# Performance work log

Hardware: AMD Instinct MI355X
Metric: run time of the kernel (lower is better)

Reference implementation:

```python
import jax, jax.numpy as jnp
import numpy as np


def setup_inputs() -> dict:
    key = jax.random.key(0)
    k1, k2, k3 = jax.random.split(key, 3)
    B, S, D, N = 2, 2048, 1024, 16
    H = D // N  # head_dim = 64
    x = jax.random.normal(k1, (B, S, D), dtype=jnp.float32)
    W_qkv = jax.random.normal(k2, (N, D, 3 * H), dtype=jnp.float32) / np.sqrt(D).astype(np.float32)
    W_out = jax.random.normal(k3, (N, H, D), dtype=jnp.float32) / np.sqrt(D).astype(np.float32)
    return {"x": x, "W_qkv": W_qkv, "W_out": W_out}


def reference(x, W_qkv, W_out):
    B, S, D = x.shape
    head_dim = W_qkv.shape[-1] // 3
    # QKV projection per head: [B, N, S, 3*H]
    qkv = jnp.einsum('bsd,ndh->bnsh', x, W_qkv)
    q, k, v = jnp.split(qkv, 3, axis=-1)  # each [B, N, S, H]
    scale = jnp.asarray(1.0 / np.sqrt(head_dim), dtype=x.dtype)
    attn = jnp.einsum('bnqh,bnkh->bnqk', q, k) * scale  # [B, N, S, S]
    # causal mask: -1e10 above the diagonal (matches buffer in original)
    mask = jnp.asarray(-1e10, dtype=x.dtype) * (1.0 - jnp.tril(jnp.ones((S, S), dtype=x.dtype)))
    attn = jax.nn.softmax(attn + mask, axis=-1)
    out = jnp.einsum('bnqk,bnkh->bnqh', attn, v)  # [B, N, S, H]
    # faithful to original: raw row-major reshape [B,N,S,H] -> [B, N*H, S]
    out = out.reshape(B, -1, S)
    # faithful to original einsum: d kept, n and h summed over W_out
    return jnp.einsum('bds,nhd->bsd', out, W_out)
```

## Files before the change

kernel.cpp:

```cpp
#include <hip/hip_runtime.h>
#include <hip/hip_bf16.h>

#define B_ 2
#define S_ 2048
#define D_ 1024
#define N_ 16
#define H_ 64

typedef unsigned short u16;
typedef unsigned int u32;
typedef __bf16 bf16x8 __attribute__((ext_vector_type(8)));
typedef u16 u16x8 __attribute__((ext_vector_type(8)));
typedef u32 u32x2 __attribute__((ext_vector_type(2)));
typedef u32 u32x4 __attribute__((ext_vector_type(4)));
typedef float f4v __attribute__((ext_vector_type(4)));

__device__ __forceinline__ u16 f2b(float f) {
    u32 u = __builtin_bit_cast(u32, f);
    u32 r = (u + 0x7FFFu + ((u >> 16) & 1u)) >> 16;
    return (u16)r;
}
__device__ __forceinline__ bf16x8 asbf(u16x8 v) { return __builtin_bit_cast(bf16x8, v); }
__device__ __forceinline__ u32 cvtpk(float a, float b) {
    u32 r;
    asm("v_cvt_pk_bf16_f32 %0, %1, %2" : "=v"(r) : "v"(a), "v"(b));
    return r;
}
__device__ __forceinline__ void gload16(const u16* g, u16* l) {
    __builtin_amdgcn_global_load_lds((const __attribute__((address_space(1))) void*)g,
                                     (__attribute__((address_space(3))) void*)l, 16, 0, 0);
}

__global__ __launch_bounds__(256) void k_setup(const float* __restrict__ x,
                                               const float* __restrict__ w,
                                               const float* __restrict__ Wout,
                                               u16* __restrict__ xb,
                                               u16* __restrict__ wt,
                                               float* __restrict__ wsum) {
    __shared__ float T[64][65];
    const int bid = blockIdx.x;
    const int t = threadIdx.x;
    if (bid < 2048) {
        size_t i = ((size_t)bid * 256 + t) * 8;
        float4 f0 = *(const float4*)(x + i);
        float4 f1 = *(const float4*)(x + i + 4);
        u16x8 o;
        o[0] = f2b(f0.x); o[1] = f2b(f0.y); o[2] = f2b(f0.z); o[3] = f2b(f0.w);
        o[4] = f2b(f1.x); o[5] = f2b(f1.y); o[6] = f2b(f1.z); o[7] = f2b(f1.w);
        *(u16x8*)(xb + i) = o;
    } else if (bid < 2816) {
        const int v = bid - 2048;
        const int n = v / 48, rem = v % 48;
        const int jt = rem >> 4, d0 = (rem & 15) * 64;
        const int j0 = jt * 64;
        const float sc = (jt == 0) ? 0.125f * 1.44269504089f : 1.0f;
#pragma unroll
        for (int rep = 0; rep < 4; ++rep) {
            int vv = t + rep * 256;
            int row = vv >> 4, c4 = vv & 15;
            float4 f = *(const float4*)(w + ((size_t)(n * 1024 + d0 + row)) * 192 + j0 + c4 * 4);
            T[row][c4 * 4 + 0] = f.x * sc;
            T[row][c4 * 4 + 1] = f.y * sc;
            T[row][c4 * 4 + 2] = f.z * sc;
            T[row][c4 * 4 + 3] = f.w * sc;
        }
        __syncthreads();
#pragma unroll
        for (int rep = 0; rep < 2; ++rep) {
            int c = t + rep * 256;
            int j = c >> 3, db = c & 7;
            u16x8 o;
#pragma unroll
            for (int e = 0; e < 8; ++e) o[e] = f2b(T[db * 8 + e][j]);
            *(u16x8*)(wt + ((size_t)(n * 192 + j0 + j)) * 1024 + d0 + db * 8) = o;
        }
    } else {
        const int bx = bid - 2816;
        const int dd = t & 15, rr = t >> 4;
        const int d = bx * 16 + dd;
        float s = 0.f;
        for (int r = rr * 64; r < rr * 64 + 64; ++r) s += Wout[(size_t)r * 1024 + d];
        float* red = &T[0][0];
        red[rr * 17 + dd] = s;
        __syncthreads();
        if (rr == 0) {
            float tt = 0.f;
#pragma unroll
            for (int k = 0; k < 16; ++k) tt += red[k * 17 + dd];
            wsum[d] = tt;
        }
    }
}

__global__ __launch_bounds__(512) void k_qkv(const u16* __restrict__ xb,
                                             const u16* __restrict__ wt,
                                             u16* __restrict__ qbuf,
                                             u16* __restrict__ kbuf,
                                             u16* __restrict__ vt) {
    __shared__ u16 As[128 * 64];
    __shared__ u16 Bst[192 * 64];
    const int st = blockIdx.x, n = blockIdx.y;
    const int t = threadIdx.x;
    const int w = t >> 6, lane = t & 63, hi2 = lane >> 4, lo4 = lane & 15;
    const int wm = w >> 2, wn = w & 3;

    const int l8 = lane >> 3, l7 = (lane & 7) * 8;
    const u16* AgL = xb + (size_t)(st * 128 + w * 16 + l8) * 1024 + l7;
    u16* AdL = As + w * 16 * 64;
    const u16* BgL = wt + (size_t)(n * 192 + w * 24 + l8) * 1024 + l7;
    u16* BdL = Bst + w * 24 * 64;

    f4v acc[4][3];
#pragma unroll
    for (int i = 0; i < 4; ++i)
#pragma unroll
        for (int j = 0; j < 3; ++j) acc[i][j] = (f4v){0.f, 0.f, 0.f, 0.f};

    for (int kk = 0; kk < 16; ++kk) {
        __syncthreads();
        const int ko = kk * 64;
        gload16(AgL + ko, AdL);
        gload16(AgL + ko + (size_t)8 * 1024, AdL + 8 * 64);
        gload16(BgL + ko, BdL);
        gload16(BgL + ko + (size_t)8 * 1024, BdL + 8 * 64);
        gload16(BgL + ko + (size_t)16 * 1024, BdL + 16 * 64);
        __syncthreads();
        bf16x8 fa[4][2];
#pragma unroll
        for (int ms = 0; ms < 4; ++ms) {
            const u16* ar = As + (wm * 64 + ms * 16 + lo4) * 64;
            fa[ms][0] = asbf(*(const u16x8*)(ar + hi2 * 8));
            fa[ms][1] = asbf(*(const u16x8*)(ar + hi2 * 8 + 32));
        }
        __builtin_amdgcn_s_setprio(1);
#pragma unroll
        for (int fj = 0; fj < 3; ++fj) {
            const u16* br = Bst + (wn * 48 + fj * 16 + lo4) * 64;
            bf16x8 fb0 = asbf(*(const u16x8*)(br + hi2 * 8));
            bf16x8 fb1 = asbf(*(const u16x8*)(br + hi2 * 8 + 32));
#pragma unroll
            for (int ms = 0; ms < 4; ++ms) {
                acc[ms][fj] = __builtin_amdgcn_mfma_f32_16x16x32_bf16(fa[ms][0], fb0, acc[ms][fj], 0, 0, 0);
                acc[ms][fj] = __builtin_amdgcn_mfma_f32_16x16x32_bf16(fa[ms][1], fb1, acc[ms][fj], 0, 0, 0);
            }
        }
        __builtin_amdgcn_s_setprio(0);
    }

    const int b = st >> 4, s128 = (st & 15) * 128;
    u16* Cs = As;
#pragma unroll
    for (int sec = 0; sec < 3; ++sec) {
        __syncthreads();
#pragma unroll
        for (int fj = 0; fj < 3; ++fj) {
            const int base = wn * 48 + fj * 16;
            if ((base >> 6) == sec) {
                const int col = base - sec * 64 + lo4;
#pragma unroll
                for (int ms = 0; ms < 4; ++ms)
#pragma unroll
                    for (int r = 0; r < 4; ++r)
                        Cs[(wm * 64 + ms * 16 + hi2 * 4 + r) * 64 + col] = f2b(acc[ms][fj][r]);
            }
        }
        __syncthreads();
        if (sec == 2) {
            const int h = t & 63, sb = t >> 6;
            u16x8 o0, o1;
#pragma unroll
            for (int e = 0; e < 8; ++e) o0[e] = Cs[(sb * 16 + e) * 64 + h];
#pragma unroll
            for (int e = 0; e < 8; ++e) o1[e] = Cs[(sb * 16 + 8 + e) * 64 + h];
            u16* dst = vt + ((size_t)(b * 16 + n) * 64 + h) * 2048 + s128 + sb * 16;
            *(u16x8*)dst = o0;
            *(u16x8*)(dst + 8) = o1;
        } else {
            const int row = t >> 2, off = (t & 3) * 16;
            u16* dst = (sec == 0) ? qbuf : kbuf;
            dst += ((size_t)(b * 16 + n) * 2048 + s128 + row) * 64 + off;
            *(u16x8*)dst = *(const u16x8*)(Cs + row * 64 + off);
            *(u16x8*)(dst + 8) = *(const u16x8*)(Cs + row * 64 + off + 8);
        }
    }
}

__global__ __launch_bounds__(512) void k_attn(const u16* __restrict__ qbuf,
                                              const u16* __restrict__ kbuf,
                                              const u16* __restrict__ vt,
                                              const float* __restrict__ wsum,
                                              float* __restrict__ out) {
    __shared__ u16 SMEM[16384];
    u16* Ks = SMEM;
    u16* Vs = SMEM + 8192;
    const int id = blockIdx.x;
    const int bn = id & 31;
    const int qx = id >> 5;
    const int qb = (qx < 8) ? (15 - 2 * qx) : (2 * (qx - 8));
    const int t = threadIdx.x;
    const int w = t >> 6, lane = t & 63, hi2 = lane >> 4, lo4 = lane & 15;

    const int q = qb * 128 + w * 16 + lo4;
    const u16* Qp = qbuf + ((size_t)bn * 2048 + q) * 64;
    bf16x8 bq0 = asbf(*(const u16x8*)(Qp + hi2 * 8));
    bf16x8 bq1 = asbf(*(const u16x8*)(Qp + 32 + hi2 * 8));

    const int srow = t >> 3, so = t & 7;
    const u16* Kg = kbuf + (size_t)bn * 2048 * 64 + (size_t)srow * 64 + so * 8;
    const u16* Vg = vt + (size_t)bn * 64 * 2048 + (size_t)srow * 2048 + so * 8;
    const int ssw = (srow & 7) << 3;
    const int ksoff = srow * 64 + ((so * 8) ^ ssw);
    const int vsb = 32 * (so >> 2) + 16 * (so & 1) + 4 * ((so >> 1) & 1);
    const int vo0 = srow * 64 + ((vsb + 0) ^ ssw);
    const int vo1 = srow * 64 + ((vsb + 8) ^ ssw);

    f4v accO[4];
#pragma unroll
    for (int i = 0; i < 4; ++i) accO[i] = (f4v){0.f, 0.f, 0.f, 0.f};
    float l = 0.f;

    const int rsw = (lo4 & 7) << 3;
    const int npair = qb + 1;

    u16x8 krA = *(const u16x8*)(Kg);
    u16x8 krB = *(const u16x8*)(Kg + 4096);
    u16x8 vrA = *(const u16x8*)(Vg);
    u16x8 vrB = *(const u16x8*)(Vg + 64);

    for (int pair = 0; pair < npair; ++pair) {
        __syncthreads();
        *(u16x8*)(Ks + ksoff) = krA;
        *(u16x8*)(Ks + 4096 + ksoff) = krB;
        {
            u32x4 va = __builtin_bit_cast(u32x4, vrA);
            u32x4 vb = __builtin_bit_cast(u32x4, vrB);
            *(u32x2*)(Vs + vo0) = (u32x2){va[0], va[1]};
            *(u32x2*)(Vs + vo1) = (u32x2){va[2], va[3]};
            *(u32x2*)(Vs + 4096 + vo0) = (u32x2){vb[0], vb[1]};
            *(u32x2*)(Vs + 4096 + vo1) = (u32x2){vb[2], vb[3]};
        }
        if (pair + 1 < npair) {
            const size_t ko = (size_t)(pair + 1) * 8192;
            krA = *(const u16x8*)(Kg + ko);
            krB = *(const u16x8*)(Kg + ko + 4096);
            vrA = *(const u16x8*)(Vg + (pair + 1) * 128);
            vrB = *(const u16x8*)(Vg + (pair + 1) * 128 + 64);
        }
        __syncthreads();

#pragma unroll
        for (int sub = 0; sub < 2; ++sub) {
            const int kb = 2 * pair + sub;
            const u16* Kc = Ks + sub * 4096;
            const u16* Vc = Vs + sub * 4096;

            f4v s4[4];
#pragma unroll
            for (int i = 0; i < 4; ++i) s4[i] = (f4v){0.f, 0.f, 0.f, 0.f};
            __builtin_amdgcn_s_setprio(1);
#pragma unroll
            for (int fi = 0; fi < 4; ++fi) {
                const u16* kr = Kc + (fi * 16 + lo4) * 64;
                bf16x8 ka0 = asbf(*(const u16x8*)(kr + ((hi2 * 8) ^ rsw)));
                bf16x8 ka1 = asbf(*(const u16x8*)(kr + ((hi2 * 8 + 32) ^ rsw)));
                s4[fi] = __builtin_amdgcn_mfma_f32_16x16x32_bf16(ka0, bq0, s4[fi], 0, 0, 0);
                s4[fi] = __builtin_amdgcn_mfma_f32_16x16x32_bf16(ka1, bq1, s4[fi], 0, 0, 0);
            }
            __builtin_amdgcn_s_setprio(0);

            if (kb >= 2 * qb) {
#pragma unroll
                for (int fi = 0; fi < 4; ++fi)
#pragma unroll
                    for (int r = 0; r < 4; ++r) {
                        int kvg = kb * 64 + fi * 16 + hi2 * 4 + r;
                        if (kvg > q) s4[fi][r] = -3.0e38f;
                    }
            }

#pragma unroll
            for (int fi = 0; fi < 4; ++fi)
#pragma unroll
                for (int r = 0; r < 4; ++r) {
                    float pv = __builtin_exp2f(s4[fi][r]);
                    s4[fi][r] = pv;
                    l += pv;
                }

            u32x4 p0 = {cvtpk(s4[0][0], s4[0][1]), cvtpk(s4[0][2], s4[0][3]),
                        cvtpk(s4[1][0], s4[1][1]), cvtpk(s4[1][2], s4[1][3])};
            u32x4 p1 = {cvtpk(s4[2][0], s4[2][1]), cvtpk(s4[2][2], s4[2][3]),
                        cvtpk(s4[3][0], s4[3][1]), cvtpk(s4[3][2], s4[3][3])};
            bf16x8 pb0 = __builtin_bit_cast(bf16x8, p0);
            bf16x8 pb1 = __builtin_bit_cast(bf16x8, p1);

            __builtin_amdgcn_s_setprio(1);
#pragma unroll
            for (int fh = 0; fh < 4; ++fh) {
                const u16* vrw = Vc + (fh * 16 + lo4) * 64;
                bf16x8 va0 = asbf(*(const u16x8*)(vrw + ((hi2 * 8) ^ rsw)));
                bf16x8 va1 = asbf(*(const u16x8*)(vrw + ((32 + hi2 * 8) ^ rsw)));
                accO[fh] = __builtin_amdgcn_mfma_f32_16x16x32_bf16(va0, pb0, accO[fh], 0, 0, 0);
                accO[fh] = __builtin_amdgcn_mfma_f32_16x16x32_bf16(va1, pb1, accO[fh], 0, 0, 0);
            }
            __builtin_amdgcn_s_setprio(0);
        }
    }

    l += __shfl_xor(l, 16);
    l += __shfl_xor(l, 32);

    __syncthreads();
    float* Osh = (float*)SMEM;
    {
        float inv = 1.f / l;
        const int orl = w * 16 + lo4;
        const int osw = (lo4 & 7) << 2;
        float* Or = Osh + orl * 64;
#pragma unroll
        for (int fh = 0; fh < 4; ++fh) {
            f4v o;
#pragma unroll
            for (int r = 0; r < 4; ++r) o[r] = accO[fh][r] * inv;
            *(f4v*)(Or + ((fh * 16 + hi2 * 4) ^ osw)) = o;
        }
    }
    __syncthreads();
    {
        const int b = bn >> 4, n = bn & 15;
        const int d0 = n * 64 + qb * 4;
        float4 wv = *(const float4*)(wsum + d0);
#pragma unroll
        for (int rep = 0; rep < 4; ++rep) {
            int p = rep * 512 + t;
            int h = p & 63, tt = p >> 6;
            const int key = (tt & 7) << 2;
            const int hc = h ^ key;
            float4 o;
            o.x = Osh[(tt)*64 + hc] * wv.x;
            o.y = Osh[(32 + tt) * 64 + hc] * wv.y;
            o.z = Osh[(64 + tt) * 64 + hc] * wv.z;
            o.w = Osh[(96 + tt) * 64 + hc] * wv.w;
            *(float4*)(out + ((size_t)b * 2048 + p) * 1024 + d0) = o;
        }
    }
}

extern "C" void kernel_launch(void* const* d_in, const int* in_sizes, int n_in,
                              void* d_out, int out_size, void* d_ws, size_t ws_size,
                              hipStream_t stream) {
    const float* x = (const float*)d_in[0];
    const float* Wqkv = (const float*)d_in[1];
    const float* Wout = (const float*)d_in[2];
    float* out = (float*)d_out;

    char* p = (char*)d_ws;
    float* wsum = (float*)p; p += 4096;
    u16* xb = (u16*)p; p += (size_t)4096 * 1024 * 2;
    u16* wt = (u16*)p; p += (size_t)16 * 192 * 1024 * 2;
    u16* qb_ = (u16*)p; p += (size_t)32 * 2048 * 64 * 2;
    u16* kb_ = (u16*)p; p += (size_t)32 * 2048 * 64 * 2;
    u16* vt_ = (u16*)p; p += (size_t)32 * 2048 * 64 * 2;

    k_setup<<<2880, 256, 0, stream>>>(x, Wqkv, Wout, xb, wt, wsum);
    k_qkv<<<dim3(32, 16), 512, 0, stream>>>(xb, wt, qb_, kb_, vt_);
    k_attn<<<512, 512, 0, stream>>>(qb_, kb_, vt_, wsum, out);
}
```

Measured before the change: 88.82 us.

## Use atomic work queue with 64-row query tiles in attention kernel

The attention kernel now uses 256-thread blocks that each own 64 query rows instead of 512-thread blocks over 128 rows. Blocks pull work units from a global atomic counter, ordered longest-causal-first, and loop until the queue is empty. The counter is reset inside the setup kernel. This aims to balance the triangular causal workload across CUs and raise occupancy. In exchange it adds an atomic and extra barriers per unit, and K/V tiles are reloaded by twice as many blocks.

New measurement: 113.9 us. +28.2%, slower.

```diff
diff --git a/kernel.cpp b/kernel.cpp
--- a/kernel.cpp
+++ b/kernel.cpp
@@ -36,11 +36,13 @@
                                                const float* __restrict__ Wout,
                                                u16* __restrict__ xb,
                                                u16* __restrict__ wt,
-                                               float* __restrict__ wsum) {
+                                               float* __restrict__ wsum,
+                                               u32* __restrict__ ctr) {
     __shared__ float T[64][65];
     const int bid = blockIdx.x;
     const int t = threadIdx.x;
     if (bid < 2048) {
+        if (bid == 0 && t == 0) ctr[0] = 0u;
         size_t i = ((size_t)bid * 256 + t) * 8;
         float4 f0 = *(const float4*)(x + i);
         float4 f1 = *(const float4*)(x + i + 4);
@@ -185,163 +187,193 @@
     }
 }
 
-__global__ __launch_bounds__(512) void k_attn(const u16* __restrict__ qbuf,
-                                              const u16* __restrict__ kbuf,
-                                              const u16* __restrict__ vt,
-                                              const float* __restrict__ wsum,
-                                              float* __restrict__ out) {
+__global__ __launch_bounds__(256, 4) void k_attn(const u16* __restrict__ qbuf,
+                                                 const u16* __restrict__ kbuf,
+                                                 const u16* __restrict__ vt,
+                                                 const float* __restrict__ wsum,
+                                                 float* __restrict__ out,
+                                                 u32* __restrict__ ctr) {
     __shared__ u16 SMEM[16384];
+    __shared__ u32 unit_s;
     u16* Ks = SMEM;
     u16* Vs = SMEM + 8192;
-    const int id = blockIdx.x;
-    const int bn = id & 31;
-    const int qx = id >> 5;
-    const int qb = (qx < 8) ? (15 - 2 * qx) : (2 * (qx - 8));
     const int t = threadIdx.x;
     const int w = t >> 6, lane = t & 63, hi2 = lane >> 4, lo4 = lane & 15;
-
-    const int q = qb * 128 + w * 16 + lo4;
-    const u16* Qp = qbuf + ((size_t)bn * 2048 + q) * 64;
-    bf16x8 bq0 = asbf(*(const u16x8*)(Qp + hi2 * 8));
-    bf16x8 bq1 = asbf(*(const u16x8*)(Qp + 32 + hi2 * 8));
-
-    const int srow = t >> 3, so = t & 7;
-    const u16* Kg = kbuf + (size_t)bn * 2048 * 64 + (size_t)srow * 64 + so * 8;
-    const u16* Vg = vt + (size_t)bn * 64 * 2048 + (size_t)srow * 2048 + so * 8;
+    const int rsw = (lo4 & 7) << 3;
+
+    const int srow = t >> 2, q4 = t & 3;
     const int ssw = (srow & 7) << 3;
-    const int ksoff = srow * 64 + ((so * 8) ^ ssw);
-    const int vsb = 32 * (so >> 2) + 16 * (so & 1) + 4 * ((so >> 1) & 1);
-    const int vo0 = srow * 64 + ((vsb + 0) ^ ssw);
-    const int vo1 = srow * 64 + ((vsb + 8) ^ ssw);
-
-    f4v accO[4];
-#pragma unroll
-    for (int i = 0; i < 4; ++i) accO[i] = (f4v){0.f, 0.f, 0.f, 0.f};
-    float l = 0.f;
-
-    const int rsw = (lo4 & 7) << 3;
-    const int npair = qb + 1;
-
-    u16x8 krA = *(const u16x8*)(Kg);
-    u16x8 krB = *(const u16x8*)(Kg + 4096);
-    u16x8 vrA = *(const u16x8*)(Vg);
-    u16x8 vrB = *(const u16x8*)(Vg + 64);
-
-    for (int pair = 0; pair < npair; ++pair) {
-        __syncthreads();
-        *(u16x8*)(Ks + ksoff) = krA;
-        *(u16x8*)(Ks + 4096 + ksoff) = krB;
+    const int ko0 = srow * 64 + ((q4 * 16) ^ ssw);
+    const int ko1 = srow * 64 + ((q4 * 16 + 8) ^ ssw);
+    const int soA = q4 * 2, soB = q4 * 2 + 1;
+    const int vsbA = 32 * (soA >> 2) + 16 * (soA & 1) + 4 * ((soA >> 1) & 1);
+    const int vsbB = 32 * (soB >> 2) + 16 * (soB & 1) + 4 * ((soB >> 1) & 1);
+    const int voA0 = srow * 64 + ((vsbA + 0) ^ ssw);
+    const int voA1 = srow * 64 + ((vsbA + 8) ^ ssw);
+    const int voB0 = srow * 64 + ((vsbB + 0) ^ ssw);
+    const int voB1 = srow * 64 + ((vsbB + 8) ^ ssw);
+
+    for (;;) {
+        __syncthreads();
+        if (t == 0) unit_s = atomicAdd(ctr, 1u);
+        __syncthreads();
+        const u32 unit = unit_s;
+        if (unit >= 1024u) return;
+        const int bn = (int)(unit & 31u);
+        const int qt = 31 - (int)(unit >> 5);
+
+        const int q = qt * 64 + w * 16 + lo4;
+        const u16* Qp = qbuf + ((size_t)bn * 2048 + q) * 64;
+        bf16x8 bq0 = asbf(*(const u16x8*)(Qp + hi2 * 8));
+        bf16x8 bq1 = asbf(*(const u16x8*)(Qp + 32 + hi2 * 8));
+
+        const u16* Kg = kbuf + (size_t)bn * 131072 + (size_t)srow * 64 + q4 * 16;
+        const u16* Vg = vt + (size_t)bn * 131072 + (size_t)srow * 2048 + q4 * 16;
+
+        f4v accO[4];
+#pragma unroll
+        for (int i = 0; i < 4; ++i) accO[i] = (f4v){0.f, 0.f, 0.f, 0.f};
+        float l = 0.f;
+        const int nkb = qt + 1;
+        const int npair = (nkb + 1) >> 1;
+
+        u16x8 krA0 = *(const u16x8*)(Kg);
+        u16x8 krA1 = *(const u16x8*)(Kg + 8);
+        u16x8 krB0 = *(const u16x8*)(Kg + 4096);
+        u16x8 krB1 = *(const u16x8*)(Kg + 4096 + 8);
+        u16x8 vrA0 = *(const u16x8*)(Vg);
+        u16x8 vrA1 = *(const u16x8*)(Vg + 8);
+        u16x8 vrB0 = *(const u16x8*)(Vg + 64);
+        u16x8 vrB1 = *(const u16x8*)(Vg + 64 + 8);
+
+        for (int pair = 0; pair < npair; ++pair) {
+            __syncthreads();
+            *(u16x8*)(Ks + ko0) = krA0;
+            *(u16x8*)(Ks + ko1) = krA1;
+            *(u16x8*)(Ks + 4096 + ko0) = krB0;
+            *(u16x8*)(Ks + 4096 + ko1) = krB1;
+            {
+                u32x4 a0 = __builtin_bit_cast(u32x4, vrA0);
+                u32x4 a1 = __builtin_bit_cast(u32x4, vrA1);
+                u32x4 b0 = __builtin_bit_cast(u32x4, vrB0);
+                u32x4 b1 = __builtin_bit_cast(u32x4, vrB1);
+                *(u32x2*)(Vs + voA0) = (u32x2){a0[0], a0[1]};
+                *(u32x2*)(Vs + voA1) = (u32x2){a0[2], a0[3]};
+                *(u32x2*)(Vs + voB0) = (u32x2){a1[0], a1[1]};
+                *(u32x2*)(Vs + voB1) = (u32x2){a1[2], a1[3]};
+                *(u32x2*)(Vs + 4096 + voA0) = (u32x2){b0[0], b0[1]};
+                *(u32x2*)(Vs + 4096 + voA1) = (u32x2){b0[2], b0[3]};
+                *(u32x2*)(Vs + 4096 + voB0) = (u32x2){b1[0], b1[1]};
+                *(u32x2*)(Vs + 4096 + voB1) = (u32x2){b1[2], b1[3]};
+            }
+            if (pair + 1 < npair) {
+                const size_t ko = (size_t)(pair + 1) * 8192;
+                const int vo = (pair + 1) * 128;
+                krA0 = *(const u16x8*)(Kg + ko);
+                krA1 = *(const u16x8*)(Kg + ko + 8);
+                krB0 = *(const u16x8*)(Kg + ko + 4096);
+                krB1 = *(const u16x8*)(Kg + ko + 4096 + 8);
+                vrA0 = *(const u16x8*)(Vg + vo);
+                vrA1 = *(const u16x8*)(Vg + vo + 8);
+                vrB0 = *(const u16x8*)(Vg + vo + 64);
+                vrB1 = *(const u16x8*)(Vg + vo + 64 + 8);
+            }
+            __syncthreads();
+
+#pragma unroll
+            for (int sub = 0; sub < 2; ++sub) {
+                const int kb = 2 * pair + sub;
+                if (kb < nkb) {
+                    const u16* Kc = Ks + sub * 4096;
+                    const u16* Vc = Vs + sub * 4096;
+
+                    f4v s4[4];
+#pragma unroll
+                    for (int i = 0; i < 4; ++i) s4[i] = (f4v){0.f, 0.f, 0.f, 0.f};
+                    __builtin_amdgcn_s_setprio(1);
+#pragma unroll
+                    for (int fi = 0; fi < 4; ++fi) {
+                        const u16* kr = Kc + (fi * 16 + lo4) * 64;
+                        bf16x8 ka0 = asbf(*(const u16x8*)(kr + ((hi2 * 8) ^ rsw)));
+                        bf16x8 ka1 = asbf(*(const u16x8*)(kr + ((hi2 * 8 + 32) ^ rsw)));
+                        s4[fi] = __builtin_amdgcn_mfma_f32_16x16x32_bf16(ka0, bq0, s4[fi], 0, 0, 0);
+                        s4[fi] = __builtin_amdgcn_mfma_f32_16x16x32_bf16(ka1, bq1, s4[fi], 0, 0, 0);
+                    }
+                    __builtin_amdgcn_s_setprio(0);
+
+                    if (kb == qt) {
+#pragma unroll
+                        for (int fi = 0; fi < 4; ++fi)
+#pragma unroll
+                            for (int r = 0; r < 4; ++r) {
+                                int kvg = kb * 64 + fi * 16 + hi2 * 4 + r;
+                                if (kvg > q) s4[fi][r] = -3.0e38f;
+                            }
+                    }
+
+#pragma unroll
+                    for (int fi = 0; fi < 4; ++fi)
+#pragma unroll
+                        for (int r = 0; r < 4; ++r) {
+                            float pv = __builtin_exp2f(s4[fi][r]);
+                            s4[fi][r] = pv;
+                            l += pv;
+                        }
+
+                    u32x4 p0 = {cvtpk(s4[0][0], s4[0][1]), cvtpk(s4[0][2], s4[0][3]),
+                                cvtpk(s4[1][0], s4[1][1]), cvtpk(s4[1][2], s4[1][3])};
+                    u32x4 p1 = {cvtpk(s4[2][0], s4[2][1]), cvtpk(s4[2][2], s4[2][3]),
+                                cvtpk(s4[3][0], s4[3][1]), cvtpk(s4[3][2], s4[3][3])};
+                    bf16x8 pb0 = __builtin_bit_cast(bf16x8, p0);
+                    bf16x8 pb1 = __builtin_bit_cast(bf16x8, p1);
+
+                    __builtin_amdgcn_s_setprio(1);
+#pragma unroll
+                    for (int fh = 0; fh < 4; ++fh) {
+                        const u16* vrw = Vc + (fh * 16 + lo4) * 64;
+                        bf16x8 va0 = asbf(*(const u16x8*)(vrw + ((hi2 * 8) ^ rsw)));
+                        bf16x8 va1 = asbf(*(const u16x8*)(vrw + ((32 + hi2 * 8) ^ rsw)));
+                        accO[fh] = __builtin_amdgcn_mfma_f32_16x16x32_bf16(va0, pb0, accO[fh], 0, 0, 0);
+                        accO[fh] = __builtin_amdgcn_mfma_f32_16x16x32_bf16(va1, pb1, accO[fh], 0, 0, 0);
+                    }
+                    __builtin_amdgcn_s_setprio(0);
+                }
+            }
+        }
+
+        l += __shfl_xor(l, 16);
+        l += __shfl_xor(l, 32);
+
+        __syncthreads();
+        float* Osh = (float*)SMEM;
         {
-            u32x4 va = __builtin_bit_cast(u32x4, vrA);
-            u32x4 vb = __builtin_bit_cast(u32x4, vrB);
-            *(u32x2*)(Vs + vo0) = (u32x2){va[0], va[1]};
-            *(u32x2*)(Vs + vo1) = (u32x2){va[2], va[3]};
-            *(u32x2*)(Vs + 4096 + vo0) = (u32x2){vb[0], vb[1]};
-            *(u32x2*)(Vs + 4096 + vo1) = (u32x2){vb[2], vb[3]};
-        }
-        if (pair + 1 < npair) {
-            const size_t ko = (size_t)(pair + 1) * 8192;
-            krA = *(const u16x8*)(Kg + ko);
-            krB = *(const u16x8*)(Kg + ko + 4096);
-            vrA = *(const u16x8*)(Vg + (pair + 1) * 128);
-            vrB = *(const u16x8*)(Vg + (pair + 1) * 128 + 64);
-        }
-        __syncthreads();
-
-#pragma unroll
-        for (int sub = 0; sub < 2; ++sub) {
-            const int kb = 2 * pair + sub;
-            const u16* Kc = Ks + sub * 4096;
-            const u16* Vc = Vs + sub * 4096;
-
-            f4v s4[4];
-#pragma unroll
-            for (int i = 0; i < 4; ++i) s4[i] = (f4v){0.f, 0.f, 0.f, 0.f};
-            __builtin_amdgcn_s_setprio(1);
-#pragma unroll
-            for (int fi = 0; fi < 4; ++fi) {
-                const u16* kr = Kc + (fi * 16 + lo4) * 64;
-                bf16x8 ka0 = asbf(*(const u16x8*)(kr + ((hi2 * 8) ^ rsw)));
-                bf16x8 ka1 = asbf(*(const u16x8*)(kr + ((hi2 * 8 + 32) ^ rsw)));
-                s4[fi] = __builtin_amdgcn_mfma_f32_16x16x32_bf16(ka0, bq0, s4[fi], 0, 0, 0);
-                s4[fi] = __builtin_amdgcn_mfma_f32_16x16x32_bf16(ka1, bq1, s4[fi], 0, 0, 0);
-            }
-            __builtin_amdgcn_s_setprio(0);
-
-            if (kb >= 2 * qb) {
-#pragma unroll
-                for (int fi = 0; fi < 4; ++fi)
-#pragma unroll
-                    for (int r = 0; r < 4; ++r) {
-                        int kvg = kb * 64 + fi * 16 + hi2 * 4 + r;
-                        if (kvg > q) s4[fi][r] = -3.0e38f;
-                    }
-            }
-
-#pragma unroll
-            for (int fi = 0; fi < 4; ++fi)
-#pragma unroll
-                for (int r = 0; r < 4; ++r) {
-                    float pv = __builtin_exp2f(s4[fi][r]);
-                    s4[fi][r] = pv;
-                    l += pv;
-                }
-
-            u32x4 p0 = {cvtpk(s4[0][0], s4[0][1]), cvtpk(s4[0][2], s4[0][3]),
-                        cvtpk(s4[1][0], s4[1][1]), cvtpk(s4[1][2], s4[1][3])};
-            u32x4 p1 = {cvtpk(s4[2][0], s4[2][1]), cvtpk(s4[2][2], s4[2][3]),
-                        cvtpk(s4[3][0], s4[3][1]), cvtpk(s4[3][2], s4[3][3])};
-            bf16x8 pb0 = __builtin_bit_cast(bf16x8, p0);
-            bf16x8 pb1 = __builtin_bit_cast(bf16x8, p1);
-
-            __builtin_amdgcn_s_setprio(1);
+            float inv = 1.f / l;
+            const int orl = w * 16 + lo4;
+            const int osw = (lo4 & 7) << 2;
+            float* Or = Osh + orl * 64;
 #pragma unroll
             for (int fh = 0; fh < 4; ++fh) {
-                const u16* vrw = Vc + (fh * 16 + lo4) * 64;
-                bf16x8 va0 = asbf(*(const u16x8*)(vrw + ((hi2 * 8) ^ rsw)));
-                bf16x8 va1 = asbf(*(const u16x8*)(vrw + ((32 + hi2 * 8) ^ rsw)));
-                accO[fh] = __builtin_amdgcn_mfma_f32_16x16x32_bf16(va0, pb0, accO[fh], 0, 0, 0);
-                accO[fh] = __builtin_amdgcn_mfma_f32_16x16x32_bf16(va1, pb1, accO[fh], 0, 0, 0);
-            }
-            __builtin_amdgcn_s_setprio(0);
-        }
-    }
-
-    l += __shfl_xor(l, 16);
-    l += __shfl_xor(l, 32);
-
-    __syncthreads();
-    float* Osh = (float*)SMEM;
-    {
-        float inv = 1.f / l;
-        const int orl = w * 16 + lo4;
-        const int osw = (lo4 & 7) << 2;
-        float* Or = Osh + orl * 64;
-#pragma unroll
-        for (int fh = 0; fh < 4; ++fh) {
-            f4v o;
-#pragma unroll
-            for (int r = 0; r < 4; ++r) o[r] = accO[fh][r] * inv;
-            *(f4v*)(Or + ((fh * 16 + hi2 * 4) ^ osw)) = o;
-        }
-    }
-    __syncthreads();
-    {
-        const int b = bn >> 4, n = bn & 15;
-        const int d0 = n * 64 + qb * 4;
-        float4 wv = *(const float4*)(wsum + d0);
-#pragma unroll
-        for (int rep = 0; rep < 4; ++rep) {
-            int p = rep * 512 + t;
-            int h = p & 63, tt = p >> 6;
-            const int key = (tt & 7) << 2;
-            const int hc = h ^ key;
-            float4 o;
-            o.x = Osh[(tt)*64 + hc] * wv.x;
-            o.y = Osh[(32 + tt) * 64 + hc] * wv.y;
-            o.z = Osh[(64 + tt) * 64 + hc] * wv.z;
-            o.w = Osh[(96 + tt) * 64 + hc] * wv.w;
-            *(float4*)(out + ((size_t)b * 2048 + p) * 1024 + d0) = o;
+                f4v o;
+#pragma unroll
+                for (int r = 0; r < 4; ++r) o[r] = accO[fh][r] * inv;
+                *(f4v*)(Or + ((fh * 16 + hi2 * 4) ^ osw)) = o;
+            }
+        }
+        __syncthreads();
+        {
+            const int b = bn >> 4, n = bn & 15;
+            const int d0 = n * 64 + qt * 2;
+            const float wx = wsum[d0], wy = wsum[d0 + 1];
+#pragma unroll
+            for (int rep = 0; rep < 8; ++rep) {
+                int p = rep * 256 + t;
+                int h = p & 63, tt = p >> 6;
+                const int key = (tt & 7) << 2;
+                const int hc = h ^ key;
+                float2 o = make_float2(Osh[tt * 64 + hc] * wx,
+                                       Osh[(32 + tt) * 64 + hc] * wy);
+                *(float2*)(out + ((size_t)b * 2048 + p) * 1024 + d0) = o;
+            }
         }
     }
 }
@@ -356,13 +388,14 @@
 
     char* p = (char*)d_ws;
     float* wsum = (float*)p; p += 4096;
+    u32* ctr = (u32*)p; p += 4096;
     u16* xb = (u16*)p; p += (size_t)4096 * 1024 * 2;
     u16* wt = (u16*)p; p += (size_t)16 * 192 * 1024 * 2;
     u16* qb_ = (u16*)p; p += (size_t)32 * 2048 * 64 * 2;
     u16* kb_ = (u16*)p; p += (size_t)32 * 2048 * 64 * 2;
     u16* vt_ = (u16*)p; p += (size_t)32 * 2048 * 64 * 2;
 
-    k_setup<<<2880, 256, 0, stream>>>(x, Wqkv, Wout, xb, wt, wsum);
+    k_setup<<<2880, 256, 0, stream>>>(x, Wqkv, Wout, xb, wt, wsum, ctr);
     k_qkv<<<dim3(32, 16), 512, 0, stream>>>(xb, wt, qb_, kb_, vt_);
-    k_attn<<<512, 512, 0, stream>>>(qb_, kb_, vt_, wsum, out);
-}
+    k_attn<<<1024, 256, 0, stream>>>(qb_, kb_, vt_, wsum, out, ctr);
+}
```

## Split attention KV range across two blocks and combine partials via atomic flag

Applied to the files above, without the earlier changes.

Each query block's key range is split into two halves handled by separate workgroups (1024 blocks instead of 512). Each half writes partial O (bf16) and row sums to workspace, and the last-arriving block, detected by an atomic counter, merges them and runs the epilogue. This targets load imbalance and low parallelism from causal attention with 512 blocks. It adds partial-result traffic, bf16 rounding of the partial accumulators, a counter reset in the setup kernel, and an occupancy hint on launch bounds.

Measured after the change: 323.0 us. 3.64x slower.

```diff
diff --git a/kernel.cpp b/kernel.cpp
--- a/kernel.cpp
+++ b/kernel.cpp
@@ -26,6 +26,8 @@
     asm("v_cvt_pk_bf16_f32 %0, %1, %2" : "=v"(r) : "v"(a), "v"(b));
     return r;
 }
+__device__ __forceinline__ float blo(u32 p) { return __builtin_bit_cast(float, p << 16); }
+__device__ __forceinline__ float bhi(u32 p) { return __builtin_bit_cast(float, p & 0xFFFF0000u); }
 __device__ __forceinline__ void gload16(const u16* g, u16* l) {
     __builtin_amdgcn_global_load_lds((const __attribute__((address_space(1))) void*)g,
                                      (__attribute__((address_space(3))) void*)l, 16, 0, 0);
@@ -36,11 +38,13 @@
                                                const float* __restrict__ Wout,
                                                u16* __restrict__ xb,
                                                u16* __restrict__ wt,
-                                               float* __restrict__ wsum) {
+                                               float* __restrict__ wsum,
+                                               u32* __restrict__ done) {
     __shared__ float T[64][65];
     const int bid = blockIdx.x;
     const int t = threadIdx.x;
     if (bid < 2048) {
+        if (bid == 0) { done[t] = 0u; done[t + 256] = 0u; }
         size_t i = ((size_t)bid * 256 + t) * 8;
         float4 f0 = *(const float4*)(x + i);
         float4 f1 = *(const float4*)(x + i + 4);
@@ -185,18 +189,23 @@
     }
 }
 
-__global__ __launch_bounds__(512) void k_attn(const u16* __restrict__ qbuf,
-                                              const u16* __restrict__ kbuf,
-                                              const u16* __restrict__ vt,
-                                              const float* __restrict__ wsum,
-                                              float* __restrict__ out) {
+__global__ __launch_bounds__(512, 8) void k_attn(const u16* __restrict__ qbuf,
+                                                 const u16* __restrict__ kbuf,
+                                                 const u16* __restrict__ vt,
+                                                 const float* __restrict__ wsum,
+                                                 float* __restrict__ out,
+                                                 u32* __restrict__ pO,
+                                                 float* __restrict__ pl,
+                                                 u32* __restrict__ done) {
     __shared__ u16 SMEM[16384];
+    __shared__ u32 flag_s;
     u16* Ks = SMEM;
     u16* Vs = SMEM + 8192;
-    const int id = blockIdx.x;
-    const int bn = id & 31;
-    const int qx = id >> 5;
-    const int qb = (qx < 8) ? (15 - 2 * qx) : (2 * (qx - 8));
+    const int u = blockIdx.x;
+    const int qb = (u < 512) ? (15 - (u >> 5)) : ((u - 512) >> 5);
+    const int bn = u & 31;
+    const int hh = (u >= 512) ? 1 : 0;
+    const int uid = qb * 32 + bn;
     const int t = threadIdx.x;
     const int w = t >> 6, lane = t & 63, hi2 = lane >> 4, lo4 = lane & 15;
 
@@ -206,8 +215,8 @@
     bf16x8 bq1 = asbf(*(const u16x8*)(Qp + 32 + hi2 * 8));
 
     const int srow = t >> 3, so = t & 7;
-    const u16* Kg = kbuf + (size_t)bn * 2048 * 64 + (size_t)srow * 64 + so * 8;
-    const u16* Vg = vt + (size_t)bn * 64 * 2048 + (size_t)srow * 2048 + so * 8;
+    const u16* Kg = kbuf + (size_t)bn * 131072 + (size_t)srow * 64 + so * 8;
+    const u16* Vg = vt + (size_t)bn * 131072 + (size_t)srow * 2048 + so * 8;
     const int ssw = (srow & 7) << 3;
     const int ksoff = srow * 64 + ((so * 8) ^ ssw);
     const int vsb = 32 * (so >> 2) + 16 * (so & 1) + 4 * ((so >> 1) & 1);
@@ -220,12 +229,14 @@
     float l = 0.f;
 
     const int rsw = (lo4 & 7) << 3;
-    const int npair = qb + 1;
-
-    u16x8 krA = *(const u16x8*)(Kg);
-    u16x8 krB = *(const u16x8*)(Kg + 4096);
-    u16x8 vrA = *(const u16x8*)(Vg);
-    u16x8 vrB = *(const u16x8*)(Vg + 64);
+    const int base = hh * (qb + 1);
+    const int count = qb + 1;
+    const int npair = (count + 1) >> 1;
+
+    u16x8 krA = *(const u16x8*)(Kg + (size_t)base * 4096);
+    u16x8 krB = *(const u16x8*)(Kg + (size_t)(base + 1) * 4096);
+    u16x8 vrA = *(const u16x8*)(Vg + base * 64);
+    u16x8 vrB = *(const u16x8*)(Vg + (base + 1) * 64);
 
     for (int pair = 0; pair < npair; ++pair) {
         __syncthreads();
@@ -240,73 +251,107 @@
             *(u32x2*)(Vs + 4096 + vo1) = (u32x2){vb[2], vb[3]};
         }
         if (pair + 1 < npair) {
-            const size_t ko = (size_t)(pair + 1) * 8192;
-            krA = *(const u16x8*)(Kg + ko);
-            krB = *(const u16x8*)(Kg + ko + 4096);
-            vrA = *(const u16x8*)(Vg + (pair + 1) * 128);
-            vrB = *(const u16x8*)(Vg + (pair + 1) * 128 + 64);
+            const int tb = base + 2 * pair + 2;
+            krA = *(const u16x8*)(Kg + (size_t)tb * 4096);
+            krB = *(const u16x8*)(Kg + (size_t)(tb + 1) * 4096);
+            vrA = *(const u16x8*)(Vg + tb * 64);
+            vrB = *(const u16x8*)(Vg + (tb + 1) * 64);
         }
         __syncthreads();
 
 #pragma unroll
         for (int sub = 0; sub < 2; ++sub) {
-            const int kb = 2 * pair + sub;
-            const u16* Kc = Ks + sub * 4096;
-            const u16* Vc = Vs + sub * 4096;
-
-            f4v s4[4];
-#pragma unroll
-            for (int i = 0; i < 4; ++i) s4[i] = (f4v){0.f, 0.f, 0.f, 0.f};
-            __builtin_amdgcn_s_setprio(1);
-#pragma unroll
-            for (int fi = 0; fi < 4; ++fi) {
-                const u16* kr = Kc + (fi * 16 + lo4) * 64;
-                bf16x8 ka0 = asbf(*(const u16x8*)(kr + ((hi2 * 8) ^ rsw)));
-                bf16x8 ka1 = asbf(*(const u16x8*)(kr + ((hi2 * 8 + 32) ^ rsw)));
-                s4[fi] = __builtin_amdgcn_mfma_f32_16x16x32_bf16(ka0, bq0, s4[fi], 0, 0, 0);
-                s4[fi] = __builtin_amdgcn_mfma_f32_16x16x32_bf16(ka1, bq1, s4[fi], 0, 0, 0);
+            const int krel = 2 * pair + sub;
+            if (krel < count) {
+                const int kb = base + krel;
+                const u16* Kc = Ks + sub * 4096;
+                const u16* Vc = Vs + sub * 4096;
+
+                f4v s4[4];
+#pragma unroll
+                for (int i = 0; i < 4; ++i) s4[i] = (f4v){0.f, 0.f, 0.f, 0.f};
+                __builtin_amdgcn_s_setprio(1);
+#pragma unroll
+                for (int fi = 0; fi < 4; ++fi) {
+                    const u16* kr = Kc + (fi * 16 + lo4) * 64;
+                    bf16x8 ka0 = asbf(*(const u16x8*)(kr + ((hi2 * 8) ^ rsw)));
+                    bf16x8 ka1 = asbf(*(const u16x8*)(kr + ((hi2 * 8 + 32) ^ rsw)));
+                    s4[fi] = __builtin_amdgcn_mfma_f32_16x16x32_bf16(ka0, bq0, s4[fi], 0, 0, 0);
+                    s4[fi] = __builtin_amdgcn_mfma_f32_16x16x32_bf16(ka1, bq1, s4[fi], 0, 0, 0);
+                }
+                __builtin_amdgcn_s_setprio(0);
+
+                if (kb >= 2 * qb) {
+#pragma unroll
+                    for (int fi = 0; fi < 4; ++fi)
+#pragma unroll
+                        for (int r = 0; r < 4; ++r) {
+                            int kvg = kb * 64 + fi * 16 + hi2 * 4 + r;
+                            if (kvg > q) s4[fi][r] = -3.0e38f;
+                        }
+                }
+
+#pragma unroll
+                for (int fi = 0; fi < 4; ++fi)
+#pragma unroll
+                    for (int r = 0; r < 4; ++r) {
+                        float pv = __builtin_exp2f(s4[fi][r]);
+                        s4[fi][r] = pv;
+                        l += pv;
+                    }
+
+                u32x4 p0 = {cvtpk(s4[0][0], s4[0][1]), cvtpk(s4[0][2], s4[0][3]),
+                            cvtpk(s4[1][0], s4[1][1]), cvtpk(s4[1][2], s4[1][3])};
+                u32x4 p1 = {cvtpk(s4[2][0], s4[2][1]), cvtpk(s4[2][2], s4[2][3]),
+                            cvtpk(s4[3][0], s4[3][1]), cvtpk(s4[3][2], s4[3][3])};
+                bf16x8 pb0 = __builtin_bit_cast(bf16x8, p0);
+                bf16x8 pb1 = __builtin_bit_cast(bf16x8, p1);
+
+                __builtin_amdgcn_s_setprio(1);
+#pragma unroll
+                for (int fh = 0; fh < 4; ++fh) {
+                    const u16* vrw = Vc + (fh * 16 + lo4) * 64;
+                    bf16x8 va0 = asbf(*(const u16x8*)(vrw + ((hi2 * 8) ^ rsw)));
+                    bf16x8 va1 = asbf(*(const u16x8*)(vrw + ((32 + hi2 * 8) ^ rsw)));
+                    accO[fh] = __builtin_amdgcn_mfma_f32_16x16x32_bf16(va0, pb0, accO[fh], 0, 0, 0);
+                    accO[fh] = __builtin_amdgcn_mfma_f32_16x16x32_bf16(va1, pb1, accO[fh], 0, 0, 0);
+                }
+                __builtin_amdgcn_s_setprio(0);
             }
-            __builtin_amdgcn_s_setprio(0);
-
-            if (kb >= 2 * qb) {
-#pragma unroll
-                for (int fi = 0; fi < 4; ++fi)
-#pragma unroll
-                    for (int r = 0; r < 4; ++r) {
-                        int kvg = kb * 64 + fi * 16 + hi2 * 4 + r;
-                        if (kvg > q) s4[fi][r] = -3.0e38f;
-                    }
-            }
-
-#pragma unroll
-            for (int fi = 0; fi < 4; ++fi)
-#pragma unroll
-                for (int r = 0; r < 4; ++r) {
-                    float pv = __builtin_exp2f(s4[fi][r]);
-                    s4[fi][r] = pv;
-                    l += pv;
-                }
-
-            u32x4 p0 = {cvtpk(s4[0][0], s4[0][1]), cvtpk(s4[0][2], s4[0][3]),
-                        cvtpk(s4[1][0], s4[1][1]), cvtpk(s4[1][2], s4[1][3])};
-            u32x4 p1 = {cvtpk(s4[2][0], s4[2][1]), cvtpk(s4[2][2], s4[2][3]),
-                        cvtpk(s4[3][0], s4[3][1]), cvtpk(s4[3][2], s4[3][3])};
-            bf16x8 pb0 = __builtin_bit_cast(bf16x8, p0);
-            bf16x8 pb1 = __builtin_bit_cast(bf16x8, p1);
-
-            __builtin_amdgcn_s_setprio(1);
-#pragma unroll
-            for (int fh = 0; fh < 4; ++fh) {
-                const u16* vrw = Vc + (fh * 16 + lo4) * 64;
-                bf16x8 va0 = asbf(*(const u16x8*)(vrw + ((hi2 * 8) ^ rsw)));
-                bf16x8 va1 = asbf(*(const u16x8*)(vrw + ((32 + hi2 * 8) ^ rsw)));
-                accO[fh] = __builtin_amdgcn_mfma_f32_16x16x32_bf16(va0, pb0, accO[fh], 0, 0, 0);
-                accO[fh] = __builtin_amdgcn_mfma_f32_16x16x32_bf16(va1, pb1, accO[fh], 0, 0, 0);
-            }
-            __builtin_amdgcn_s_setprio(0);
-        }
-    }
-
+        }
+    }
+
+    u32 own[8];
+#pragma unroll
+    for (int fh = 0; fh < 4; ++fh) {
+        own[fh * 2 + 0] = cvtpk(accO[fh][0], accO[fh][1]);
+        own[fh * 2 + 1] = cvtpk(accO[fh][2], accO[fh][3]);
+    }
+    u32* myO = pO + ((size_t)(uid * 2 + hh)) * 4096 + (w * 64 + lane) * 8;
+#pragma unroll
+    for (int e = 0; e < 8; e += 2) *(u32x2*)(myO + e) = (u32x2){own[e], own[e + 1]};
+    pl[(uid * 2 + hh) * 512 + w * 64 + lane] = l;
+
+    __syncthreads();
+    if (t == 0) {
+        __threadfence();
+        flag_s = atomicAdd(&done[uid], 1u);
+    }
+    __syncthreads();
+    if (flag_s == 0u) return;
+    __threadfence();
+
+    const u32* prO = pO + ((size_t)(uid * 2 + (1 - hh))) * 4096 + (w * 64 + lane) * 8;
+    float lp = pl[(uid * 2 + (1 - hh)) * 512 + w * 64 + lane];
+#pragma unroll
+    for (int fh = 0; fh < 4; ++fh) {
+        u32x2 pq = *(const u32x2*)(prO + fh * 2);
+        accO[fh][0] = blo(own[fh * 2 + 0]) + blo(pq[0]);
+        accO[fh][1] = bhi(own[fh * 2 + 0]) + bhi(pq[0]);
+        accO[fh][2] = blo(own[fh * 2 + 1]) + blo(pq[1]);
+        accO[fh][3] = bhi(own[fh * 2 + 1]) + bhi(pq[1]);
+    }
+    l += lp;
     l += __shfl_xor(l, 16);
     l += __shfl_xor(l, 32);
 
@@ -356,13 +401,16 @@
 
     char* p = (char*)d_ws;
     float* wsum = (float*)p; p += 4096;
+    u32* done = (u32*)p; p += 4096;
     u16* xb = (u16*)p; p += (size_t)4096 * 1024 * 2;
     u16* wt = (u16*)p; p += (size_t)16 * 192 * 1024 * 2;
     u16* qb_ = (u16*)p; p += (size_t)32 * 2048 * 64 * 2;
     u16* kb_ = (u16*)p; p += (size_t)32 * 2048 * 64 * 2;
     u16* vt_ = (u16*)p; p += (size_t)32 * 2048 * 64 * 2;
-
-    k_setup<<<2880, 256, 0, stream>>>(x, Wqkv, Wout, xb, wt, wsum);
+    u32* pO = (u32*)p; p += (size_t)1024 * 4096 * 4;
+    float* pl = (float*)p; p += (size_t)1024 * 512 * 4;
+
+    k_setup<<<2880, 256, 0, stream>>>(x, Wqkv, Wout, xb, wt, wsum, done);
     k_qkv<<<dim3(32, 16), 512, 0, stream>>>(xb, wt, qb_, kb_, vt_);
-    k_attn<<<512, 512, 0, stream>>>(qb_, kb_, vt_, wsum, out);
-}
+    k_attn<<<1024, 512, 0, stream>>>(qb_, kb_, vt_, wsum, out, pO, pl, done);
+}
```
